# Kernel optimization log

Hardware: AMD Instinct MI355X
Metric: run time of the kernel (lower is better)

Reference implementation:

```python
import jax, jax.numpy as jnp
import numpy as np

NUM_EXPERTS = 64
NUM_SELECTED = 2
HASH_BITS = 32


def setup_inputs() -> dict:
    key = jax.random.key(0)
    k1, k2 = jax.random.split(key)
    hidden_states = jax.random.normal(k1, (4, 4096, 2048), dtype=jnp.float32)
    # torch Linear weight [out_features, in_features], init normal(std=0.01), bias zeros
    hash_w = jax.random.normal(k2, (NUM_SELECTED * HASH_BITS, 2048), dtype=jnp.float32) * 0.01
    hash_b = jnp.zeros((NUM_SELECTED * HASH_BITS,), dtype=jnp.float32)
    return {"hidden_states": hidden_states, "hash_w": hash_w, "hash_b": hash_b}


def reference(hidden_states, hash_w, hash_b):
    B, S, H = hidden_states.shape
    T = B * S
    x = hidden_states.reshape(T, H)
    # hash projection: [T, k*32]
    h = x @ hash_w.T + hash_b
    bits = (h > 0).astype(jnp.int32).reshape(T, NUM_SELECTED, HASH_BITS)
    cand = bits.sum(axis=-1) % NUM_EXPERTS  # [T, k] candidate expert per slot

    # Sequential dedup (vectorized over tokens): for each slot i in order, if the
    # candidate collides with an already-chosen expert for that token, advance
    # (e+1) % E until a free expert is found (always exists since k <= E).
    used = jnp.zeros((T, NUM_EXPERTS), dtype=bool)
    offs = jnp.arange(NUM_EXPERTS)
    chosen = []
    for i in range(NUM_SELECTED):
        e = cand[:, i]  # [T]
        pos = (e[:, None] + offs[None, :]) % NUM_EXPERTS  # [T, E] probe sequence
        probed = jnp.take_along_axis(used, pos, axis=1)  # [T, E] used flags along probe
        off = jnp.argmax(~probed, axis=1)  # first free offset (0 if candidate free)
        ne = (e + off) % NUM_EXPERTS
        used = used | jax.nn.one_hot(ne, NUM_EXPERTS, dtype=bool)
        chosen.append(ne)
    expert_indices = jnp.stack(chosen, axis=1).astype(jnp.int32)  # [T, k]
    expert_weights = jnp.full((T, NUM_SELECTED), 1.0 / NUM_SELECTED, dtype=jnp.float32)
    router_logits = jnp.zeros((T, NUM_EXPERTS), dtype=jnp.float32)
    return expert_weights, expert_indices, router_logits
```

## Files before the change

kernel.cpp:

```cpp
#include <hip/hip_runtime.h>


constexpr int H_DIM  = 2048;
constexpr int NJ     = 64;
constexpr int TOK    = 32;
constexpr int KC     = 64;
constexpr int NCHUNK = H_DIM / KC;
constexpr int XF     = TOK * KC;
constexpr int WF     = NJ * KC;
constexpr int BUF    = XF + WF;
constexpr int XSLOTS = XF / 4;
constexpr int NTHR   = 512;
constexpr int SLOTS  = BUF / 4;

__device__ __forceinline__ int sw_of(int row) {
    return (3 * (row >> 3) + ((row >> 2) & 1)) & 7;
}

__device__ __forceinline__ void stage_chunk(const float* __restrict__ x,
                                            const float* __restrict__ w,
                                            float* smem, int fb,
                                            int tok0, int k0, int tid) {
#pragma unroll
    for (int it = 0; it < SLOTS / NTHR; ++it) {
        const int slot = it * NTHR + tid;
        const float* g;
        if (slot < XSLOTS) {
            const int row = slot >> 4, c4p = slot & 15;
            g = x + (size_t)(tok0 + row) * H_DIM + k0 + ((c4p ^ sw_of(row)) << 2);
        } else {
            const int s2 = slot - XSLOTS;
            const int row = s2 >> 4, c4p = s2 & 15;
            g = w + (size_t)row * H_DIM + k0 + ((c4p ^ sw_of(row)) << 2);
        }
        __builtin_amdgcn_global_load_lds(
            (const __attribute__((address_space(1))) void*)g,
            (__attribute__((address_space(3))) void*)(smem + fb + slot * 4),
            16, 0, 0);
    }
}

__global__ __launch_bounds__(NTHR, 4) void hash_router_kernel(
    const float* __restrict__ x,
    const float* __restrict__ w,
    const float* __restrict__ b,
    float* __restrict__ out,
    int T)
{
    __shared__ float smem[2 * BUF];
    __shared__ unsigned int bitw[TOK][2];

    const int tid = threadIdx.x;
    const int og  = tid & 7;
    const int tg  = (tid >> 3) & 3;
    const int kg  = tid >> 5;
    const int tok0 = blockIdx.x * TOK;

    if (tid < TOK * 2) ((unsigned int*)bitw)[tid] = 0u;

    float acc[8][8];
#pragma unroll
    for (int i = 0; i < 8; ++i)
#pragma unroll
        for (int j = 0; j < 8; ++j) acc[i][j] = 0.f;

    stage_chunk(x, w, smem, 0, tok0, 0, tid);

    for (int ch = 0; ch < NCHUNK; ++ch) {
        __builtin_amdgcn_s_waitcnt(0x0f70);
        __syncthreads();
        if (ch + 1 < NCHUNK)
            stage_chunk(x, w, smem, ((ch + 1) & 1) * BUF, tok0, (ch + 1) * KC, tid);

        const int fb = (ch & 1) * BUF;
        const int k4 = kg;
        float4 xv[8];
#pragma unroll
        for (int i = 0; i < 8; ++i) {
            const int row = tg * 8 + i;
            xv[i] = *(const float4*)(smem + fb + row * KC + ((k4 ^ sw_of(row)) << 2));
        }
#pragma unroll
        for (int j = 0; j < 8; ++j) {
            const int row = og * 8 + j;
            const float4 wv = *(const float4*)(smem + fb + XF + row * KC + ((k4 ^ sw_of(row)) << 2));
#pragma unroll
            for (int i = 0; i < 8; ++i) {
                acc[i][j] += xv[i].x * wv.x;
                acc[i][j] += xv[i].y * wv.y;
                acc[i][j] += xv[i].z * wv.z;
                acc[i][j] += xv[i].w * wv.w;
            }
        }
    }

    __syncthreads();
#pragma unroll
    for (int i = 0; i < 8; ++i)
#pragma unroll
        for (int j = 0; j < 8; ++j)
            acc[i][j] += __shfl_xor(acc[i][j], 32, 64);

    const int v  = tid >> 6;
    const bool lo = (tid & 32) == 0;
    const int s  = tid & 31;
    const int sw = s & 7;
#define ACC_PACK(f4) make_float4(acc[(f4) >> 1][((f4) & 1) * 4],     \
                                 acc[(f4) >> 1][((f4) & 1) * 4 + 1], \
                                 acc[(f4) >> 1][((f4) & 1) * 4 + 2], \
                                 acc[(f4) >> 1][((f4) & 1) * 4 + 3])
#define ACC_ADD(f4, val) { acc[(f4) >> 1][((f4) & 1) * 4]     += (val).x; \
                           acc[(f4) >> 1][((f4) & 1) * 4 + 1] += (val).y; \
                           acc[(f4) >> 1][((f4) & 1) * 4 + 2] += (val).z; \
                           acc[(f4) >> 1][((f4) & 1) * 4 + 3] += (val).w; }
    if (v >= 4 && lo) {
        float* base = smem + ((v - 4) * 32 + s) * 64;
#pragma unroll
        for (int f4 = 0; f4 < 16; ++f4) *(float4*)(base + ((f4 ^ sw) << 2)) = ACC_PACK(f4);
    }
    __syncthreads();
    if (v < 4 && lo) {
        const float* base = smem + (v * 32 + s) * 64;
#pragma unroll
        for (int f4 = 0; f4 < 16; ++f4) { float4 t = *(const float4*)(base + ((f4 ^ sw) << 2)); ACC_ADD(f4, t); }
    }
    __syncthreads();
    if ((v == 2 || v == 3) && lo) {
        float* base = smem + ((v - 2) * 32 + s) * 64;
#pragma unroll
        for (int f4 = 0; f4 < 16; ++f4) *(float4*)(base + ((f4 ^ sw) << 2)) = ACC_PACK(f4);
    }
    __syncthreads();
    if (v < 2 && lo) {
        const float* base = smem + (v * 32 + s) * 64;
#pragma unroll
        for (int f4 = 0; f4 < 16; ++f4) { float4 t = *(const float4*)(base + ((f4 ^ sw) << 2)); ACC_ADD(f4, t); }
    }
    __syncthreads();
    if (v == 1 && lo) {
        float* base = smem + s * 64;
#pragma unroll
        for (int f4 = 0; f4 < 16; ++f4) *(float4*)(base + ((f4 ^ sw) << 2)) = ACC_PACK(f4);
    }
    __syncthreads();

    if (v == 0 && lo) {
        const float* base = smem + s * 64;
#pragma unroll
        for (int f4 = 0; f4 < 16; ++f4) { float4 t = *(const float4*)(base + ((f4 ^ sw) << 2)); ACC_ADD(f4, t); }

        float bias[8];
#pragma unroll
        for (int j = 0; j < 8; ++j) bias[j] = b[og * 8 + j];

        const float TH = 5e-5f;
#pragma unroll
        for (int i = 0; i < 8; ++i) {
            unsigned int byte = 0u;
#pragma unroll
            for (int j = 0; j < 8; ++j) {
                const float hv = acc[i][j] + bias[j];
                bool pos;
                if (__builtin_expect(fabsf(hv) < TH, 0)) {
                    const float* xr = x + (size_t)(tok0 + tg * 8 + i) * H_DIM;
                    const float* wr = w + (size_t)(og * 8 + j) * H_DIM;
                    double sd = (double)bias[j];
                    for (int k = 0; k < H_DIM; ++k)
                        sd += (double)xr[k] * (double)wr[k];
                    pos = (sd > 0.0);
                } else {
                    pos = (hv > 0.0f);
                }
                byte |= (pos ? 1u : 0u) << j;
            }
            if (byte) atomicOr(&bitw[tg * 8 + i][og >> 2], byte << ((og & 3) * 8));
        }
    }
    __syncthreads();

    if (tid < TOK) {
        const int t  = tok0 + tid;
        const int c0 = __popc(bitw[tid][0]);
        const int c1 = __popc(bitw[tid][1]);
        const int i1 = c1 + ((c1 == c0) ? 1 : 0);
        float2 wq; wq.x = 0.5f; wq.y = 0.5f;
        *(float2*)(out + 2 * (size_t)t) = wq;
        float2 iq; iq.x = (float)c0; iq.y = (float)i1;
        *(float2*)(out + 2 * (size_t)T + 2 * (size_t)t) = iq;
    }

    float4 z; z.x = 0.f; z.y = 0.f; z.z = 0.f; z.w = 0.f;
    float* lbase = out + 4 * (size_t)T + (size_t)tok0 * NJ;
#pragma unroll
    for (int i = tid; i < TOK * NJ / 4; i += NTHR)
        *(float4*)(lbase + i * 4) = z;
}

extern "C" void kernel_launch(void* const* d_in, const int* in_sizes, int n_in,
                              void* d_out, int out_size, void* d_ws, size_t ws_size,
                              hipStream_t stream) {
    const float* x = (const float*)d_in[0];
    const float* w = (const float*)d_in[1];
    const float* b = (const float*)d_in[2];
    float* out = (float*)d_out;
    const int T = in_sizes[0] / H_DIM;
    const int grid = T / TOK;
    hash_router_kernel<<<dim3(grid), dim3(NTHR), 0, stream>>>(x, w, b, out, T);
}
```

Baseline: 345.8 us.

## Halve block tile to 16 tokens with 256 threads and shorten reduction

Shrinks each block to 16 tokens and 256 threads, doubling the grid and giving more blocks per CU. The k-split reduction now uses an extra intra-wave shuffle and a shorter LDS tree with fewer barriers. The bit-word scratch is aliased into the staging shared memory to save LDS. The cost is that each block reloads the full 64x2048 weight tile for half as many tokens, doubling weight traffic per token.

```diff
diff --git a/kernel.cpp b/kernel.cpp
--- a/kernel.cpp
+++ b/kernel.cpp
@@ -3,14 +3,14 @@
 
 constexpr int H_DIM  = 2048;
 constexpr int NJ     = 64;
-constexpr int TOK    = 32;
+constexpr int TOK    = 16;
 constexpr int KC     = 64;
 constexpr int NCHUNK = H_DIM / KC;
 constexpr int XF     = TOK * KC;
 constexpr int WF     = NJ * KC;
 constexpr int BUF    = XF + WF;
 constexpr int XSLOTS = XF / 4;
-constexpr int NTHR   = 512;
+constexpr int NTHR   = 256;
 constexpr int SLOTS  = BUF / 4;
 
 __device__ __forceinline__ int sw_of(int row) {
@@ -48,15 +48,13 @@
     int T)
 {
     __shared__ float smem[2 * BUF];
-    __shared__ unsigned int bitw[TOK][2];
+    unsigned int* bitw = (unsigned int*)(smem + 2048);
 
     const int tid = threadIdx.x;
     const int og  = tid & 7;
-    const int tg  = (tid >> 3) & 3;
-    const int kg  = tid >> 5;
+    const int tg  = (tid >> 3) & 1;
+    const int kg  = tid >> 4;
     const int tok0 = blockIdx.x * TOK;
-
-    if (tid < TOK * 2) ((unsigned int*)bitw)[tid] = 0u;
 
     float acc[8][8];
 #pragma unroll
@@ -98,13 +96,16 @@
 #pragma unroll
     for (int i = 0; i < 8; ++i)
 #pragma unroll
-        for (int j = 0; j < 8; ++j)
+        for (int j = 0; j < 8; ++j) {
+            acc[i][j] += __shfl_xor(acc[i][j], 16, 64);
             acc[i][j] += __shfl_xor(acc[i][j], 32, 64);
+        }
 
-    const int v  = tid >> 6;
-    const bool lo = (tid & 32) == 0;
-    const int s  = tid & 31;
-    const int sw = s & 7;
+    const int v    = tid >> 6;
+    const int lane = tid & 63;
+    const bool red = lane < 16;
+    const int s    = tid & 15;
+    const int sw   = s & 7;
 #define ACC_PACK(f4) make_float4(acc[(f4) >> 1][((f4) & 1) * 4],     \
                                  acc[(f4) >> 1][((f4) & 1) * 4 + 1], \
                                  acc[(f4) >> 1][((f4) & 1) * 4 + 2], \
@@ -113,38 +114,27 @@
                            acc[(f4) >> 1][((f4) & 1) * 4 + 1] += (val).y; \
                            acc[(f4) >> 1][((f4) & 1) * 4 + 2] += (val).z; \
                            acc[(f4) >> 1][((f4) & 1) * 4 + 3] += (val).w; }
-    if (v >= 4 && lo) {
-        float* base = smem + ((v - 4) * 32 + s) * 64;
+    if (v >= 2 && red) {
+        float* base = smem + ((v - 2) * 16 + s) * 64;
 #pragma unroll
         for (int f4 = 0; f4 < 16; ++f4) *(float4*)(base + ((f4 ^ sw) << 2)) = ACC_PACK(f4);
     }
+    if (v == 0 && lane >= 16 && lane < 48) bitw[lane - 16] = 0u;
     __syncthreads();
-    if (v < 4 && lo) {
-        const float* base = smem + (v * 32 + s) * 64;
+    if (v < 2 && red) {
+        const float* base = smem + (v * 16 + s) * 64;
 #pragma unroll
         for (int f4 = 0; f4 < 16; ++f4) { float4 t = *(const float4*)(base + ((f4 ^ sw) << 2)); ACC_ADD(f4, t); }
     }
     __syncthreads();
-    if ((v == 2 || v == 3) && lo) {
-        float* base = smem + ((v - 2) * 32 + s) * 64;
-#pragma unroll
-        for (int f4 = 0; f4 < 16; ++f4) *(float4*)(base + ((f4 ^ sw) << 2)) = ACC_PACK(f4);
-    }
-    __syncthreads();
-    if (v < 2 && lo) {
-        const float* base = smem + (v * 32 + s) * 64;
-#pragma unroll
-        for (int f4 = 0; f4 < 16; ++f4) { float4 t = *(const float4*)(base + ((f4 ^ sw) << 2)); ACC_ADD(f4, t); }
-    }
-    __syncthreads();
-    if (v == 1 && lo) {
+    if (v == 1 && red) {
         float* base = smem + s * 64;
 #pragma unroll
         for (int f4 = 0; f4 < 16; ++f4) *(float4*)(base + ((f4 ^ sw) << 2)) = ACC_PACK(f4);
     }
     __syncthreads();
 
-    if (v == 0 && lo) {
+    if (v == 0 && red) {
         const float* base = smem + s * 64;
 #pragma unroll
         for (int f4 = 0; f4 < 16; ++f4) { float4 t = *(const float4*)(base + ((f4 ^ sw) << 2)); ACC_ADD(f4, t); }
@@ -173,15 +163,15 @@
                 }
                 byte |= (pos ? 1u : 0u) << j;
             }
-            if (byte) atomicOr(&bitw[tg * 8 + i][og >> 2], byte << ((og & 3) * 8));
+            if (byte) atomicOr(&bitw[(tg * 8 + i) * 2 + (og >> 2)], byte << ((og & 3) * 8));
         }
     }
     __syncthreads();
 
     if (tid < TOK) {
         const int t  = tok0 + tid;
-        const int c0 = __popc(bitw[tid][0]);
-        const int c1 = __popc(bitw[tid][1]);
+        const int c0 = __popc(bitw[tid * 2 + 0]);
+        const int c1 = __popc(bitw[tid * 2 + 1]);
         const int i1 = c1 + ((c1 == c0) ? 1 : 0);
         float2 wq; wq.x = 0.5f; wq.y = 0.5f;
         *(float2*)(out + 2 * (size_t)t) = wq;
```

After: 344.1 us. No clear change (-0.5%).
